# Kernel optimization log

Measured on AMD Instinct MI355X. Metric: run time of the kernel, lower is better.

The kernel has to match this reference:

```python
import jax, jax.numpy as jnp
import numpy as np

DIM = 1024


def setup_inputs() -> dict:
    key = jax.random.key(0)
    ks = jax.random.split(key, 9)
    s = 1.0 / np.sqrt(DIM)
    x = jax.random.normal(ks[0], (4, 4096, DIM), dtype=jnp.float32)
    Wq = jax.random.uniform(ks[1], (DIM, DIM), jnp.float32, -s, s)
    bq = jax.random.uniform(ks[2], (DIM,), jnp.float32, -s, s)
    Wk = jax.random.uniform(ks[3], (DIM, DIM), jnp.float32, -s, s)
    bk = jax.random.uniform(ks[4], (DIM,), jnp.float32, -s, s)
    Wv = jax.random.uniform(ks[5], (DIM, DIM), jnp.float32, -s, s)
    bv = jax.random.uniform(ks[6], (DIM,), jnp.float32, -s, s)
    Wo = jax.random.uniform(ks[7], (DIM, DIM), jnp.float32, -s, s)
    bo = jax.random.uniform(ks[8], (DIM,), jnp.float32, -s, s)
    return {"x": x, "Wq": Wq, "bq": bq, "Wk": Wk, "bk": bk,
            "Wv": Wv, "bv": bv, "Wo": Wo, "bo": bo}


def reference(x, Wq, bq, Wk, bk, Wv, bv, Wo, bo):
    # x: [B, N, C]; weights stored as [C, C] (torch Linear applies x @ W.T,
    # here we store W already transposed so x @ W matches).
    scale = x.shape[-1] ** (-0.5)
    q = x @ Wq + bq                                  # [B, N, C]
    k = x @ Wk + bk
    v = x @ Wv + bv
    scores = jnp.einsum('bnc,bmc->bnm', q, k) * scale  # [B, N, N]
    attn = jax.nn.softmax(scores, axis=-1)
    out = jnp.einsum('bnm,bmc->bnc', attn, v)          # [B, N, C]
    return out @ Wo + bo
```

## Files before the change

### kernel.cpp

```cpp
#include <hip/hip_runtime.h>
#include <hip/hip_bf16.h>
#include <stdint.h>

typedef __bf16 bf16_8 __attribute__((ext_vector_type(8)));
typedef float  f32x4  __attribute__((ext_vector_type(4)));

#define GLL(g, l) __builtin_amdgcn_global_load_lds(                         \
    (__attribute__((address_space(1))) void*)(g),                           \
    (__attribute__((address_space(3))) void*)(l), 16, 0, 0)

__global__ void sniff_dtype(const uint32_t* __restrict__ x, uint32_t* __restrict__ flag)
{
    uint32_t w = x[threadIdx.x];
    uint32_t e = (w >> 23) & 0xFF;
    int isf32 = (e >= 100 && e <= 145) ? 1 : 0;
    unsigned long long m = __ballot(isf32);
    if (threadIdx.x == 0) *flag = (__popcll(m) >= 48) ? 1u : 0u;
}

__global__ __launch_bounds__(256)
void convert_to_bf16(const void* __restrict__ in, long elemOff,
                     __bf16* __restrict__ out, long n, const uint32_t* __restrict__ flag)
{
    long i = ((long)blockIdx.x * 256 + threadIdx.x) * 8;
    if (i >= n) return;
    bf16_8 o;
    if (*flag) {
        const float* p = (const float*)in + elemOff + i;
        float4 a = *(const float4*)p;
        float4 b = *(const float4*)(p + 4);
        o[0]=(__bf16)a.x; o[1]=(__bf16)a.y; o[2]=(__bf16)a.z; o[3]=(__bf16)a.w;
        o[4]=(__bf16)b.x; o[5]=(__bf16)b.y; o[6]=(__bf16)b.z; o[7]=(__bf16)b.w;
    } else {
        o = *(const bf16_8*)((const __bf16*)in + elemOff + i);
    }
    *(bf16_8*)(out + i) = o;
}

__global__ __launch_bounds__(256)
void convert_bias4(const void* b0, const void* b1, const void* b2, const void* b3,
                   __bf16* o0, __bf16* o1, __bf16* o2, __bf16* o3,
                   const uint32_t* __restrict__ flag)
{
    const void* in = (blockIdx.x == 0) ? b0 : (blockIdx.x == 1) ? b1
                   : (blockIdx.x == 2) ? b2 : b3;
    __bf16* out = (blockIdx.x == 0) ? o0 : (blockIdx.x == 1) ? o1
                : (blockIdx.x == 2) ? o2 : o3;
    long i = (long)threadIdx.x * 8;
    if (i >= 1024) return;
    bf16_8 o;
    if (*flag) {
        const float* p = (const float*)in + i;
        float4 a = *(const float4*)p;
        float4 b = *(const float4*)(p + 4);
        o[0]=(__bf16)a.x; o[1]=(__bf16)a.y; o[2]=(__bf16)a.z; o[3]=(__bf16)a.w;
        o[4]=(__bf16)b.x; o[5]=(__bf16)b.y; o[6]=(__bf16)b.z; o[7]=(__bf16)b.w;
    } else {
        o = *(const bf16_8*)((const __bf16*)in + i);
    }
    *(bf16_8*)(out + i) = o;
}

__global__ __launch_bounds__(256)
void convT_w4(const void* W0, const void* W1, const void* W2, const void* W3,
              __bf16* T0, __bf16* T1, __bf16* T2, __bf16* T3,
              const uint32_t* __restrict__ flag)
{
    const void* W = (blockIdx.z == 0) ? W0 : (blockIdx.z == 1) ? W1
                  : (blockIdx.z == 2) ? W2 : W3;
    __bf16* WT    = (blockIdx.z == 0) ? T0 : (blockIdx.z == 1) ? T1
                  : (blockIdx.z == 2) ? T2 : T3;
    __shared__ __bf16 tile[64][72];
    const int bc = blockIdx.x * 64, br = blockIdx.y * 64;
    const int c = threadIdx.x & 63, r0 = threadIdx.x >> 6;
    const bool f32 = (*flag != 0);
#pragma unroll
    for (int i = 0; i < 16; i++) {
        int r = i * 4 + r0;
        long idx = (long)(br + r) * 1024 + bc + c;
        float v = f32 ? ((const float*)W)[idx] : (float)((const __bf16*)W)[idx];
        tile[r][c] = (__bf16)v;
    }
    __syncthreads();
#pragma unroll
    for (int i = 0; i < 16; i++) {
        int r = i * 4 + r0;
        WT[(long)(bc + r) * 1024 + br + c] = tile[c][r];
    }
}

template<int BM_T, int BN_T, int GX, int GY, int GZ, int RX, int RY,
         int OUT_MODE, bool HAS_BIAS>
__global__ __launch_bounds__(512, 2)
void gemm_big(const __bf16* __restrict__ A, int lda,
              const __bf16* __restrict__ BT, int ldb,
              void* __restrict__ C, int ldc,
              const __bf16* __restrict__ bias,
              int kLen, long zCbytes, float scale,
              float* __restrict__ rowSums)
{
    constexpr int MT  = BM_T / 32;
    constexpr int NT  = BN_T / 64;
    constexpr int AG  = BM_T / 128;
    constexpr int BG  = BN_T / 128;
    constexpr int L   = AG + BG;

    constexpr int NRX = GX / RX;
    static_assert(NRX * ((GY * GZ) / RY) == 8, "regions must cover 8 XCDs");
    static_assert(RX * RY == (GX * GY * GZ) / 8, "region size = blocks/XCD");

    __shared__ __align__(16) __bf16 As[4 * BM_T * 32];
    __shared__ __align__(16) __bf16 Bs[4 * BN_T * 32];

    const int t    = threadIdx.x;
    const int wave = t >> 6;
    const int lane = t & 63;
    const int quad = lane >> 4;
    const int lrow = lane & 15;
    const int wm   = wave >> 2;
    const int wn   = wave & 3;

    const int h   = (int)blockIdx.x;
    const int xcd = h & 7;
    const int s0_ = h >> 3;
    const int bx  = (xcd % NRX) * RX + (s0_ % RX);
    const int byz = (xcd / NRX) * RY + (s0_ / RX);
    const int by  = byz % GY;
    const int bz  = byz / GY;

    const long m0  = (long)by * BM_T;
    const long n0  = (long)bx * BN_T;

    A  += (long)bz * kLen;
    BT += (long)bz * kLen;
    C   = (void*)((char*)C + (long)bz * zCbytes);

    const int sr = lane >> 2;
    const int sc = (lane & 3) ^ ((lane >> 3) & 3);
    const int sl = (lrow >> 1) & 3;

    const __bf16* aStage = A + (m0 + wave * (BM_T / 8) + sr) * (long)lda + sc * 8;
    const __bf16* bStage = BT + (n0 + wave * (BN_T / 8) + sr) * (long)ldb + sc * 8;

    f32x4 zero4 = {0.f, 0.f, 0.f, 0.f};
    f32x4 acc[MT][NT];
#pragma unroll
    for (int mt = 0; mt < MT; mt++)
#pragma unroll
        for (int nt = 0; nt < NT; nt++) acc[mt][nt] = zero4;

    auto STAGE_SLICE = [&](int slice) {
        const int slot = slice & 3;
        __bf16* aD = As + slot * (BM_T * 32) + wave * (BM_T / 8) * 32;
        __bf16* bD = Bs + slot * (BN_T * 32) + wave * (BN_T / 8) * 32;
#pragma unroll
        for (int g = 0; g < AG; g++)
            GLL(aStage + (long)g * 16 * lda, aD + g * 512);
#pragma unroll
        for (int g = 0; g < BG; g++)
            GLL(bStage + (long)g * 16 * ldb, bD + g * 512);
        aStage += 32; bStage += 32;
    };

    const int S = kLen >> 5;

    STAGE_SLICE(0);
    STAGE_SLICE(1);
    STAGE_SLICE(2);
    if constexpr (L == 4) asm volatile("s_waitcnt vmcnt(8)" ::: "memory");
    else                  asm volatile("s_waitcnt vmcnt(6)" ::: "memory");
    __builtin_amdgcn_s_barrier();
    __builtin_amdgcn_sched_barrier(0);

    for (int s = 0; s < S; s++) {
        const int slot = s & 3;
        const __bf16* slotA = As + slot * (BM_T * 32);
        const __bf16* slotB = Bs + slot * (BN_T * 32);

        bf16_8 afA[4], bfr[NT];
#pragma unroll
        for (int mt = 0; mt < 4; mt++)
            afA[mt] = *(const bf16_8*)(slotA
                        + (wm * (BM_T / 2) + mt * 16 + lrow) * 32 + (quad ^ sl) * 8);
#pragma unroll
        for (int nt = 0; nt < NT; nt++)
            bfr[nt] = *(const bf16_8*)(slotB
                        + (wn * (BN_T / 4) + nt * 16 + lrow) * 32 + (quad ^ sl) * 8);
        if (s + 3 < S) STAGE_SLICE(s + 3);

        __builtin_amdgcn_s_barrier();
        asm volatile("s_waitcnt lgkmcnt(0)" ::: "memory");
        __builtin_amdgcn_sched_barrier(0);
        __builtin_amdgcn_s_setprio(1);
#pragma unroll
        for (int mt = 0; mt < 4; mt++)
#pragma unroll
            for (int nt = 0; nt < NT; nt++)
                acc[mt][nt] = __builtin_amdgcn_mfma_f32_16x16x32_bf16(
                                  afA[mt], bfr[nt], acc[mt][nt], 0, 0, 0);
        __builtin_amdgcn_s_setprio(0);
        __builtin_amdgcn_s_barrier();
        __builtin_amdgcn_sched_barrier(0);

        bf16_8 afB[4];
#pragma unroll
        for (int mt = 0; mt < 4; mt++)
            afB[mt] = *(const bf16_8*)(slotA
                        + (wm * (BM_T / 2) + (mt + 4) * 16 + lrow) * 32 + (quad ^ sl) * 8);

        if (s + 4 <= S) {
            if constexpr (L == 4) asm volatile("s_waitcnt vmcnt(8)" ::: "memory");
            else                  asm volatile("s_waitcnt vmcnt(6)" ::: "memory");
        } else if (s + 3 == S) {
            if constexpr (L == 4) asm volatile("s_waitcnt vmcnt(4)" ::: "memory");
            else                  asm volatile("s_waitcnt vmcnt(3)" ::: "memory");
        } else if (s + 2 == S) {
            asm volatile("s_waitcnt vmcnt(0)" ::: "memory");
        }

        __builtin_amdgcn_s_barrier();
        asm volatile("s_waitcnt lgkmcnt(0)" ::: "memory");
        __builtin_amdgcn_sched_barrier(0);
        __builtin_amdgcn_s_setprio(1);
#pragma unroll
        for (int mt = 0; mt < 4; mt++)
#pragma unroll
            for (int nt = 0; nt < NT; nt++)
                acc[mt + 4][nt] = __builtin_amdgcn_mfma_f32_16x16x32_bf16(
                                      afB[mt], bfr[nt], acc[mt + 4][nt], 0, 0, 0);
        __builtin_amdgcn_s_setprio(0);
        __builtin_amdgcn_s_barrier();
        __builtin_amdgcn_sched_barrier(0);
    }

    if (OUT_MODE == 3) {
#pragma unroll
        for (int mt = 0; mt < MT; mt++) {
#pragma unroll
            for (int i = 0; i < 4; i++) {
                long row = m0 + wm * (BM_T / 2) + mt * 16 + quad * 4 + i;
                float rs = 0.f;
#pragma unroll
                for (int nt = 0; nt < NT; nt++) {
                    long col = n0 + wn * (BN_T / 4) + nt * 16 + lrow;
                    float e = exp2f(acc[mt][nt][i] * scale);
                    ((__bf16*)C)[row * (long)ldc + col] = (__bf16)e;
                    rs += e;
                }
                rs += __shfl_xor(rs, 1);
                rs += __shfl_xor(rs, 2);
                rs += __shfl_xor(rs, 4);
                rs += __shfl_xor(rs, 8);
                if (lrow == 0) atomicAdd(&rowSums[row], rs);
            }
        }
        return;
    }

#pragma unroll
    for (int mt = 0; mt < MT; mt++) {
#pragma unroll
        for (int nt = 0; nt < NT; nt++) {
#pragma unroll
            for (int i = 0; i < 4; i++) {
                long row = m0 + wm * (BM_T / 2) + mt * 16 + quad * 4 + i;
                long col = n0 + wn * (BN_T / 4) + nt * 16 + lrow;
                float v = acc[mt][nt][i] * scale;
                if (HAS_BIAS) v += (float)bias[col];
                if (OUT_MODE == 0)      ((__bf16*)C)[row * (long)ldc + col] = (__bf16)v;
                else if (OUT_MODE == 1) ((__bf16*)C)[col * (long)ldc + row] = (__bf16)v;
                else                    ((float* )C)[row * (long)ldc + col] = v;
            }
        }
    }
}

template<int BN_T, int OUT_MODE, bool HAS_BIAS>
__global__ __launch_bounds__(256)
void gemm_bt(const __bf16* __restrict__ A, int lda,
             const __bf16* __restrict__ BT, int ldb,
             void* __restrict__ C, int ldc,
             const __bf16* __restrict__ bias,
             int M, int N, int kLen, long zCbytes, float scale,
             float* __restrict__ rowSums)
{
    constexpr int NT    = (BN_T == 128) ? 4 : 2;
    constexpr int BHALF = BN_T * 32;
    __shared__ __align__(16) __bf16 As[2][2 * 128 * 32];
    __shared__ __align__(16) __bf16 Bs[2][2 * BHALF];

    const int t    = threadIdx.x;
    const int wave = t >> 6;
    const int lane = t & 63;
    const int quad = lane >> 4;
    const int lrow = lane & 15;
    const int wm   = wave >> 1;
    const int wn   = wave & 1;
    const long m0  = (long)blockIdx.y * 128;
    const long n0  = (long)blockIdx.x * BN_T;

    A  += (long)blockIdx.z * kLen;
    BT += (long)blockIdx.z * kLen;
    C   = (void*)((char*)C + (long)blockIdx.z * zCbytes);

    const int sr = lane >> 2;
    const int sc = (lane & 3) ^ ((lane >> 3) & 3);

    const __bf16* aSrc = A + (m0 + wave * 32 + sr) * (long)lda + sc * 8;
    const __bf16* bSrc = (BN_T == 128)
        ? BT + (n0 + wave * 32 + sr) * (long)ldb + sc * 8
        : BT + (n0 + wave * 16 + sr) * (long)ldb + sc * 8;
    const long a16 = 16L * lda, b16 = 16L * ldb;

    f32x4 zero4 = {0.f, 0.f, 0.f, 0.f};
    f32x4 acc[4][NT];
#pragma unroll
    for (int mt = 0; mt < 4; mt++)
#pragma unroll
        for (int nt = 0; nt < NT; nt++) acc[mt][nt] = zero4;

    const int sl = (lrow >> 1) & 3;

    auto STAGE = [&](int buf, const __bf16* aS, const __bf16* bS) {
        __bf16* aD = &As[buf][0] + wave * 1024;
        __bf16* bD = &Bs[buf][0] + wave * (BN_T == 128 ? 1024 : 512);
        GLL(aS, aD);
        GLL(aS + a16, aD + 512);
        GLL(bS, bD);
        if (BN_T == 128) GLL(bS + b16, bD + 512);
        GLL(aS + 32, aD + 4096);
        GLL(aS + a16 + 32, aD + 4096 + 512);
        GLL(bS + 32, bD + BHALF);
        if (BN_T == 128) GLL(bS + b16 + 32, bD + BHALF + 512);
    };

    auto COMPUTE = [&](int buf) {
#pragma unroll
        for (int kk = 0; kk < 2; kk++) {
            bf16_8 af[4], bfr[NT];
#pragma unroll
            for (int mt = 0; mt < 4; mt++)
                af[mt] = *(const bf16_8*)(&As[buf][0] + kk * 4096
                           + (wm * 64 + mt * 16 + lrow) * 32 + (quad ^ sl) * 8);
#pragma unroll
            for (int nt = 0; nt < NT; nt++)
                bfr[nt] = *(const bf16_8*)(&Bs[buf][0] + kk * BHALF
                           + (wn * (BN_T / 2) + nt * 16 + lrow) * 32 + (quad ^ sl) * 8);

#pragma unroll
            for (int mt = 0; mt < 4; mt++)
#pragma unroll
                for (int nt = 0; nt < NT; nt++)
                    acc[mt][nt] = __builtin_amdgcn_mfma_f32_16x16x32_bf16(
                                      af[mt], bfr[nt], acc[mt][nt], 0, 0, 0);
        }
    };

    STAGE(0, aSrc, bSrc);
    aSrc += 64; bSrc += 64;
    __syncthreads();

    int cur = 0;
    for (int k0 = 64; k0 < kLen; k0 += 64) {
        STAGE(cur ^ 1, aSrc, bSrc);
        aSrc += 64; bSrc += 64;
        COMPUTE(cur);
        __syncthreads();
        cur ^= 1;
    }
    COMPUTE(cur);

    if (OUT_MODE == 3) {
#pragma unroll
        for (int mt = 0; mt < 4; mt++) {
#pragma unroll
            for (int i = 0; i < 4; i++) {
                long row = m0 + wm * 64 + mt * 16 + quad * 4 + i;
                float rs = 0.f;
#pragma unroll
                for (int nt = 0; nt < NT; nt++) {
                    long col = n0 + wn * (BN_T / 2) + nt * 16 + lrow;
                    float e = exp2f(acc[mt][nt][i] * scale);
                    ((__bf16*)C)[row * (long)ldc + col] = (__bf16)e;
                    rs += e;
                }
                rs += __shfl_xor(rs, 1);
                rs += __shfl_xor(rs, 2);
                rs += __shfl_xor(rs, 4);
                rs += __shfl_xor(rs, 8);
                if (lrow == 0) atomicAdd(&rowSums[row], rs);
            }
        }
        return;
    }

#pragma unroll
    for (int mt = 0; mt < 4; mt++) {
#pragma unroll
        for (int nt = 0; nt < NT; nt++) {
#pragma unroll
            for (int i = 0; i < 4; i++) {
                long row = m0 + wm * 64 + mt * 16 + quad * 4 + i;
                long col = n0 + wn * (BN_T / 2) + nt * 16 + lrow;
                float v = acc[mt][nt][i] * scale;
                if (HAS_BIAS) v += (float)bias[col];
                if (OUT_MODE == 0)      ((__bf16*)C)[row * (long)ldc + col] = (__bf16)v;
                else if (OUT_MODE == 1) ((__bf16*)C)[col * (long)ldc + row] = (__bf16)v;
                else                    ((float* )C)[row * (long)ldc + col] = v;
            }
        }
    }
}

__global__ __launch_bounds__(256)
void softmax_f32_to_bf16(float* __restrict__ S)
{
    float* srow = S + (long)blockIdx.x * 4096;
    __bf16* prow = (__bf16*)srow;
    const int t  = threadIdx.x;
    const int wv = t >> 6, ln = t & 63;

    float4 vv[4];
    float m = -1e30f;
#pragma unroll
    for (int i = 0; i < 4; i++) {
        vv[i] = ((const float4*)srow)[t + i * 256];
        m = fmaxf(m, fmaxf(fmaxf(vv[i].x, vv[i].y), fmaxf(vv[i].z, vv[i].w)));
    }
#pragma unroll
    for (int o = 32; o; o >>= 1) m = fmaxf(m, __shfl_xor(m, o));
    __shared__ float redm[4];
    if (ln == 0) redm[wv] = m;
    __syncthreads();
    m = fmaxf(fmaxf(redm[0], redm[1]), fmaxf(redm[2], redm[3]));

    const float L2E = 1.4426950408889634f;
    float s = 0.f;
#pragma unroll
    for (int i = 0; i < 4; i++) {
        vv[i].x = exp2f((vv[i].x - m) * L2E);
        vv[i].y = exp2f((vv[i].y - m) * L2E);
        vv[i].z = exp2f((vv[i].z - m) * L2E);
        vv[i].w = exp2f((vv[i].w - m) * L2E);
        s += vv[i].x + vv[i].y + vv[i].z + vv[i].w;
    }
#pragma unroll
    for (int o = 32; o; o >>= 1) s += __shfl_xor(s, o);
    __shared__ float reds[4];
    if (ln == 0) reds[wv] = s;
    __syncthreads();
    s = reds[0] + reds[1] + reds[2] + reds[3];
    float inv = 1.f / s;

    __syncthreads();
#pragma unroll
    for (int i = 0; i < 4; i++) {
        long base = (long)(t + i * 256) * 4;
        prow[base + 0] = (__bf16)(vv[i].x * inv);
        prow[base + 1] = (__bf16)(vv[i].y * inv);
        prow[base + 2] = (__bf16)(vv[i].z * inv);
        prow[base + 3] = (__bf16)(vv[i].w * inv);
    }
}

__global__ __launch_bounds__(256)
void reduce2_to_bf16(const float* __restrict__ Sf, __bf16* __restrict__ ao)
{
    const long i = blockIdx.x;
    const float* p = Sf + 4096 * i + 2048;
    const int t = threadIdx.x;
    float4 a = ((const float4*)p)[t];
    float4 b = ((const float4*)(p + 1024))[t];
    __bf16* o = ao + i * 1024 + t * 4;
    o[0] = (__bf16)(a.x + b.x);
    o[1] = (__bf16)(a.y + b.y);
    o[2] = (__bf16)(a.z + b.z);
    o[3] = (__bf16)(a.w + b.w);
}

__global__ __launch_bounds__(256)
void reduce2_scaled(const float* __restrict__ part, const float* __restrict__ sums,
                    __bf16* __restrict__ ao)
{
    const long i = blockIdx.x;
    const float inv = 1.0f / sums[i];
    const float* p = part + i * 2048;
    const int t = threadIdx.x;
    float4 a = ((const float4*)p)[t];
    float4 b = ((const float4*)(p + 1024))[t];
    __bf16* o = ao + i * 1024 + t * 4;
    o[0] = (__bf16)((a.x + b.x) * inv);
    o[1] = (__bf16)((a.y + b.y) * inv);
    o[2] = (__bf16)((a.z + b.z) * inv);
    o[3] = (__bf16)((a.w + b.w) * inv);
}

__global__ void fill_const_f32(float* p, long n, float val)
{
    long i = (long)blockIdx.x * 256 + threadIdx.x;
    if (i < n) p[i] = val;
}

extern "C" void kernel_launch(void* const* d_in, const int* in_sizes, int n_in,
                              void* d_out, int out_size, void* d_ws, size_t ws_size,
                              hipStream_t stream)
{
    const void* x  = d_in[0];
    const void* Wq = d_in[1];
    const void* bq = d_in[2];
    const void* Wk = d_in[3];
    const void* bk = d_in[4];
    const void* Wv = d_in[5];
    const void* bv = d_in[6];
    const void* Wo = d_in[7];
    const void* bo = d_in[8];

    const int  Bb = 4, Nn = 4096, Cc = 1024;
    const long seqB = (long)Nn * Cc;
    const long allR = (long)Bb * Nn;

    auto pad = [](size_t b) { return (b + 255) & ~(size_t)255; };
    const size_t szW    = (size_t)Cc * Cc * 2;
    const size_t szBias = (size_t)Cc * 2;
    const size_t szSeq  = (size_t)seqB * 2;
    const size_t szAll  = (size_t)allR * Cc * 2;

    const size_t fixed = pad(256) + 4 * pad(szW) + 4 * pad(szBias) + pad(szAll);
    const size_t needB = fixed + 4 * pad(szSeq);
    const size_t needA = fixed + 4 * pad(szAll);

    dim3 blk(256);
    dim3 blk5(512);

    if (ws_size < needB) {
        float val = 3000.0f + (float)(ws_size >> 20);
        fill_const_f32<<<dim3((out_size + 255) / 256), blk, 0, stream>>>(
            (float*)d_out, out_size, val);
        return;
    }

    const bool batched = (ws_size >= needA);

    char* ws = (char*)d_ws;
    size_t off = 0;
    auto alloc = [&](size_t bytes) -> char* { char* p = ws + off; off += pad(bytes); return p; };

    uint32_t* flag = (uint32_t*)alloc(256);
    __bf16* WqT = (__bf16*)alloc(szW);
    __bf16* WkT = (__bf16*)alloc(szW);
    __bf16* WvT = (__bf16*)alloc(szW);
    __bf16* WoT = (__bf16*)alloc(szW);
    __bf16* bqc = (__bf16*)alloc(szBias);
    __bf16* bkc = (__bf16*)alloc(szBias);
    __bf16* bvc = (__bf16*)alloc(szBias);
    __bf16* boc = (__bf16*)alloc(szBias);
    __bf16* ao  = (__bf16*)alloc(szAll);
    const size_t tierSz = batched ? szAll : szSeq;
    __bf16* xc  = (__bf16*)alloc(tierSz);
    __bf16* q   = (__bf16*)alloc(tierSz);
    __bf16* k   = (__bf16*)alloc(tierSz);
    __bf16* vT  = (__bf16*)alloc(tierSz);

    sniff_dtype<<<dim3(1), dim3(64), 0, stream>>>((const uint32_t*)x, flag);
    convT_w4<<<dim3(16, 16, 4), blk, 0, stream>>>(Wq, Wk, Wv, Wo, WqT, WkT, WvT, WoT, flag);
    convert_bias4<<<dim3(4), blk, 0, stream>>>(bq, bk, bv, bo, bqc, bkc, bvc, boc, flag);

    const float scale    = 0.03125f;
    const float scaleL2E = 0.03125f * 1.4426950408889634f;

    if (batched) {
        convert_to_bf16<<<dim3(allR * Cc / 2048), blk, 0, stream>>>(x, 0, xc, allR * Cc, flag);

        gemm_big<256, 256, 4, 64, 1, 4, 8, 0, true><<<dim3(256), blk5, 0, stream>>>(
            xc, Cc, WqT, Cc, q,  Cc,  bqc, Cc, 0, 1.f, nullptr);
        gemm_big<256, 256, 4, 64, 1, 4, 8, 0, true><<<dim3(256), blk5, 0, stream>>>(
            xc, Cc, WkT, Cc, k,  Cc,  bkc, Cc, 0, 1.f, nullptr);
        gemm_big<256, 256, 4, 64, 1, 4, 8, 1, true><<<dim3(256), blk5, 0, stream>>>(
            xc, Cc, WvT, Cc, vT, (int)allR, bvc, Cc, 0, 1.f, nullptr);

        float* sums4 = (float*)xc;
        fill_const_f32<<<dim3(64), blk, 0, stream>>>(sums4, 4L * Nn, 0.f);

        __bf16* P   = (__bf16*)d_out;
        float* part = (float*)((char*)d_out + (size_t)Nn * Nn * 2);

        for (int b = 0; b < Bb; b++) {
            const __bf16* qb  = q + (long)b * seqB;
            const __bf16* kb  = k + (long)b * seqB;
            const __bf16* vTb = vT + (long)b * Nn;
            float* sums = sums4 + (long)b * Nn;

            gemm_big<256, 256, 16, 16, 1, 8, 4, 3, false><<<dim3(256), blk5, 0, stream>>>(
                qb, Cc, kb, Cc, P, Nn, nullptr, Cc, 0, scaleL2E, sums);

            gemm_big<256, 128, 8, 16, 2, 8, 4, 2, false><<<dim3(256), blk5, 0, stream>>>(
                P, Nn, vTb, (int)allR, part, 2048,
                nullptr, Nn / 2, 4096 , 1.f, nullptr);

            reduce2_scaled<<<dim3(Nn), blk, 0, stream>>>(
                part, sums, ao + (long)b * seqB);
        }

        gemm_big<256, 256, 4, 64, 1, 4, 8, 2, true><<<dim3(256), blk5, 0, stream>>>(
            ao, Cc, WoT, Cc, (float*)d_out, Cc, boc, Cc, 0, 1.f, nullptr);
    } else {
        float* S = (float*)d_out;
        for (int b = 0; b < Bb; b++) {
            convert_to_bf16<<<dim3(seqB / 2048), blk, 0, stream>>>(x, b * seqB, xc, seqB, flag);
            dim3 gProj(Cc / 64, Nn / 128);
            gemm_bt<64, 0, true><<<gProj, blk, 0, stream>>>(xc, Cc, WqT, Cc, q,  Cc, bqc, Nn, Cc, Cc, 0, 1.f, nullptr);
            gemm_bt<64, 0, true><<<gProj, blk, 0, stream>>>(xc, Cc, WkT, Cc, k,  Cc, bkc, Nn, Cc, Cc, 0, 1.f, nullptr);
            gemm_bt<64, 1, true><<<gProj, blk, 0, stream>>>(xc, Cc, WvT, Cc, vT, Nn, bvc, Nn, Cc, Cc, 0, 1.f, nullptr);

            gemm_bt<128, 2, false><<<dim3(Nn / 128, Nn / 128), blk, 0, stream>>>(
                q, Cc, k, Cc, S, Nn, nullptr, Nn, Nn, Cc, 0, scale, nullptr);

            softmax_f32_to_bf16<<<dim3(Nn), blk, 0, stream>>>(S);

            gemm_bt<128, 2, false><<<dim3(Cc / 128, Nn / 128, 2), blk, 0, stream>>>(
                (const __bf16*)S, 2 * Nn, vT, Nn, (float*)S + 2048, Nn,
                nullptr, Nn, Cc, Nn / 2, 4096, 1.f, nullptr);

            reduce2_to_bf16<<<dim3(Nn), blk, 0, stream>>>(S, ao + (long)b * seqB);
        }

        gemm_bt<128, 2, true><<<dim3(Cc / 128, (int)(allR / 128)), blk, 0, stream>>>(
            ao, Cc, WoT, Cc, (float*)d_out, Cc, boc, (int)allR, Cc, Cc, 0, 1.f, nullptr);
    }
}
```

Baseline: 768.2 us.

## Fuse QKV projections, batch attention over batch pairs, drop split-K reduction

Merges the three Q/K/V projection GEMMs into one launch over a concatenated weight (768 blocks), routing columns to q, k, or transposed v in the epilogue. Attention is processed two batches per launch via a z-dimension with per-batch strides. The PV GEMM now runs over the full key length and normalizes by the row sums in its epilogue, removing the split-K partial buffer and the separate reduce kernel. The fused QKV launch reads WqT as if it were a contiguous 3072-row Wq/Wk/Wv buffer, which holds only if the workspace places WkT and WvT directly after it. The change also trades parallelism: the PV GEMM has fewer blocks per batch and a K loop twice as long.

```diff
diff --git a/kernel.cpp b/kernel.cpp
--- a/kernel.cpp
+++ b/kernel.cpp
@@ -92,12 +92,13 @@
 template<int BM_T, int BN_T, int GX, int GY, int GZ, int RX, int RY,
          int OUT_MODE, bool HAS_BIAS>
 __global__ __launch_bounds__(512, 2)
-void gemm_big(const __bf16* __restrict__ A, int lda,
-              const __bf16* __restrict__ BT, int ldb,
-              void* __restrict__ C, int ldc,
+void gemm_big(const __bf16* __restrict__ A, int lda, long zA,
+              const __bf16* __restrict__ BT, int ldb, long zB,
+              void* __restrict__ C, int ldc, long zCbytes,
+              void* __restrict__ C2, void* __restrict__ C3, int ldT,
               const __bf16* __restrict__ bias,
-              int kLen, long zCbytes, float scale,
-              float* __restrict__ rowSums)
+              int kLen, float scale,
+              float* __restrict__ rowSums, long zSums)
 {
     constexpr int MT  = BM_T / 32;
     constexpr int NT  = BN_T / 64;
@@ -131,9 +132,10 @@
     const long m0  = (long)by * BM_T;
     const long n0  = (long)bx * BN_T;
 
-    A  += (long)bz * kLen;
-    BT += (long)bz * kLen;
+    A  += (long)bz * zA;
+    BT += (long)bz * zB;
     C   = (void*)((char*)C + (long)bz * zCbytes);
+    float* rs_base = rowSums ? rowSums + (long)bz * zSums : nullptr;
 
     const int sr = lane >> 2;
     const int sc = (lane & 3) ^ ((lane >> 3) & 3);
@@ -251,7 +253,46 @@
                 rs += __shfl_xor(rs, 2);
                 rs += __shfl_xor(rs, 4);
                 rs += __shfl_xor(rs, 8);
-                if (lrow == 0) atomicAdd(&rowSums[row], rs);
+                if (lrow == 0) atomicAdd(&rs_base[row], rs);
+            }
+        }
+        return;
+    }
+
+    if (OUT_MODE == 4) {
+#pragma unroll
+        for (int mt = 0; mt < MT; mt++) {
+#pragma unroll
+            for (int i = 0; i < 4; i++) {
+                long row = m0 + wm * (BM_T / 2) + mt * 16 + quad * 4 + i;
+                float inv = 1.0f / rs_base[row];
+#pragma unroll
+                for (int nt = 0; nt < NT; nt++) {
+                    long col = n0 + wn * (BN_T / 4) + nt * 16 + lrow;
+                    ((__bf16*)C)[row * (long)ldc + col] = (__bf16)(acc[mt][nt][i] * inv);
+                }
+            }
+        }
+        return;
+    }
+
+    if (OUT_MODE == 5) {
+        const int seg = (int)(n0 >> 10);
+        __bf16* Cqk = (seg == 0) ? (__bf16*)C : (__bf16*)C2;
+#pragma unroll
+        for (int mt = 0; mt < MT; mt++) {
+#pragma unroll
+            for (int nt = 0; nt < NT; nt++) {
+#pragma unroll
+                for (int i = 0; i < 4; i++) {
+                    long row  = m0 + wm * (BM_T / 2) + mt * 16 + quad * 4 + i;
+                    long gcol = n0 + wn * (BN_T / 4) + nt * 16 + lrow;
+                    long ccol = gcol & 1023;
+                    float v = acc[mt][nt][i];
+                    if (HAS_BIAS) v += (float)bias[gcol];
+                    if (seg < 2) Cqk[row * 1024 + ccol] = (__bf16)v;
+                    else ((__bf16*)C3)[ccol * (long)ldT + row] = (__bf16)v;
+                }
             }
         }
         return;
@@ -267,9 +308,8 @@
                 long col = n0 + wn * (BN_T / 4) + nt * 16 + lrow;
                 float v = acc[mt][nt][i] * scale;
                 if (HAS_BIAS) v += (float)bias[col];
-                if (OUT_MODE == 0)      ((__bf16*)C)[row * (long)ldc + col] = (__bf16)v;
-                else if (OUT_MODE == 1) ((__bf16*)C)[col * (long)ldc + row] = (__bf16)v;
-                else                    ((float* )C)[row * (long)ldc + col] = v;
+                if (OUT_MODE == 0) ((__bf16*)C)[row * (long)ldc + col] = (__bf16)v;
+                else               ((float* )C)[row * (long)ldc + col] = v;
             }
         }
     }
@@ -476,23 +516,6 @@
     o[1] = (__bf16)(a.y + b.y);
     o[2] = (__bf16)(a.z + b.z);
     o[3] = (__bf16)(a.w + b.w);
-}
-
-__global__ __launch_bounds__(256)
-void reduce2_scaled(const float* __restrict__ part, const float* __restrict__ sums,
-                    __bf16* __restrict__ ao)
-{
-    const long i = blockIdx.x;
-    const float inv = 1.0f / sums[i];
-    const float* p = part + i * 2048;
-    const int t = threadIdx.x;
-    float4 a = ((const float4*)p)[t];
-    float4 b = ((const float4*)(p + 1024))[t];
-    __bf16* o = ao + i * 1024 + t * 4;
-    o[0] = (__bf16)((a.x + b.x) * inv);
-    o[1] = (__bf16)((a.y + b.y) * inv);
-    o[2] = (__bf16)((a.z + b.z) * inv);
-    o[3] = (__bf16)((a.w + b.w) * inv);
 }
 
 __global__ void fill_const_f32(float* p, long n, float val)
@@ -571,38 +594,36 @@
     if (batched) {
         convert_to_bf16<<<dim3(allR * Cc / 2048), blk, 0, stream>>>(x, 0, xc, allR * Cc, flag);
 
-        gemm_big<256, 256, 4, 64, 1, 4, 8, 0, true><<<dim3(256), blk5, 0, stream>>>(
-            xc, Cc, WqT, Cc, q,  Cc,  bqc, Cc, 0, 1.f, nullptr);
-        gemm_big<256, 256, 4, 64, 1, 4, 8, 0, true><<<dim3(256), blk5, 0, stream>>>(
-            xc, Cc, WkT, Cc, k,  Cc,  bkc, Cc, 0, 1.f, nullptr);
-        gemm_big<256, 256, 4, 64, 1, 4, 8, 1, true><<<dim3(256), blk5, 0, stream>>>(
-            xc, Cc, WvT, Cc, vT, (int)allR, bvc, Cc, 0, 1.f, nullptr);
+        gemm_big<256, 256, 12, 64, 1, 6, 16, 5, true><<<dim3(768), blk5, 0, stream>>>(
+            xc, Cc, 0, WqT, Cc, 0,
+            q, Cc, 0, k, vT, (int)allR,
+            bqc, Cc, 1.f, nullptr, 0);
 
         float* sums4 = (float*)xc;
         fill_const_f32<<<dim3(64), blk, 0, stream>>>(sums4, 4L * Nn, 0.f);
 
-        __bf16* P   = (__bf16*)d_out;
-        float* part = (float*)((char*)d_out + (size_t)Nn * Nn * 2);
-
-        for (int b = 0; b < Bb; b++) {
-            const __bf16* qb  = q + (long)b * seqB;
-            const __bf16* kb  = k + (long)b * seqB;
-            const __bf16* vTb = vT + (long)b * Nn;
-            float* sums = sums4 + (long)b * Nn;
-
-            gemm_big<256, 256, 16, 16, 1, 8, 4, 3, false><<<dim3(256), blk5, 0, stream>>>(
-                qb, Cc, kb, Cc, P, Nn, nullptr, Cc, 0, scaleL2E, sums);
-
-            gemm_big<256, 128, 8, 16, 2, 8, 4, 2, false><<<dim3(256), blk5, 0, stream>>>(
-                P, Nn, vTb, (int)allR, part, 2048,
-                nullptr, Nn / 2, 4096 , 1.f, nullptr);
-
-            reduce2_scaled<<<dim3(Nn), blk, 0, stream>>>(
-                part, sums, ao + (long)b * seqB);
+        __bf16* P = (__bf16*)d_out;
+        const long Pelems = (long)Nn * Nn;
+
+        for (int pr = 0; pr < 2; pr++) {
+            const int b0 = pr * 2;
+            gemm_big<256, 256, 16, 16, 2, 8, 8, 3, false><<<dim3(512), blk5, 0, stream>>>(
+                q + (long)b0 * seqB, Cc, seqB,
+                k + (long)b0 * seqB, Cc, seqB,
+                P, Nn, (long)Pelems * 2 , nullptr, nullptr, 0,
+                nullptr, Cc, scaleL2E, sums4 + (long)b0 * Nn, Nn);
+
+            gemm_big<256, 128, 8, 16, 2, 8, 4, 4, false><<<dim3(256), blk5, 0, stream>>>(
+                P, Nn, Pelems,
+                vT + (long)b0 * Nn, (int)allR, (long)Nn,
+                ao + (long)b0 * seqB, Cc, seqB * 2 , nullptr, nullptr, 0,
+                nullptr, Nn, 1.f, sums4 + (long)b0 * Nn, Nn);
         }
 
         gemm_big<256, 256, 4, 64, 1, 4, 8, 2, true><<<dim3(256), blk5, 0, stream>>>(
-            ao, Cc, WoT, Cc, (float*)d_out, Cc, boc, Cc, 0, 1.f, nullptr);
+            ao, Cc, 0, WoT, Cc, 0,
+            (float*)d_out, Cc, 0, nullptr, nullptr, 0,
+            boc, Cc, 1.f, nullptr, 0);
     } else {
         float* S = (float*)d_out;
         for (int b = 0; b < Bb; b++) {
```

New measurement: 772.3 us. About the same (+0.5%).
